# Performance work log

Hardware: AMD Instinct MI355X
Metric: run time of the kernel (lower is better)

Reference implementation:

```python
import jax, jax.numpy as jnp
import numpy as np

NUM_NODES = 17
DIM_IN = 64
DIM_OUT = 64
B, T = 128, 300
CONNECTIONS = {10: [9], 9: [8, 10], 8: [7, 9], 14: [15, 8], 15: [16, 14],
               11: [12, 8], 12: [13, 11], 7: [0, 8], 0: [1, 7], 1: [2, 0],
               2: [3, 1], 4: [5, 0], 5: [6, 4], 16: [15], 13: [12], 3: [2], 6: [5]}

def build_adj():
    a = np.zeros((NUM_NODES, NUM_NODES), dtype=np.float32)
    for i in range(NUM_NODES):
        for j in CONNECTIONS[i]:
            a[i, j] = 1.0
    return jnp.asarray(a)

def setup_inputs() -> dict:
    key = jax.random.key(0)
    k_x, k_w, k_b = jax.random.split(key, 3)
    x = jax.random.normal(k_x, (B, T, NUM_NODES, DIM_IN), dtype=jnp.float32)
    # xavier_uniform with gain=1.414 over [2, dim_in, dim_out]
    gain = 1.414
    bound = gain * np.sqrt(6.0 / (DIM_IN + DIM_OUT))
    W = jax.random.uniform(k_w, (2, DIM_IN, DIM_OUT), minval=-bound, maxval=bound, dtype=jnp.float32)
    M = jnp.ones((NUM_NODES, DIM_OUT), dtype=jnp.float32)
    adj2 = jnp.full((NUM_NODES, NUM_NODES), 1e-6, dtype=jnp.float32)
    stdv = 1.0 / np.sqrt(DIM_OUT)
    bias = jax.random.uniform(k_b, (DIM_OUT,), minval=-stdv, maxval=stdv, dtype=jnp.float32)
    adj = build_adj()  # fixed (non-trainable) skeleton adjacency buffer
    return {"x": x, "W": W, "M": M, "adj2": adj2, "bias": bias, "adj": adj}

def reference(x, W, M, adj2, bias, adj):
    # h0, h1: [B,T,N,dout]
    h0 = jnp.einsum('btni,io->btno', x, W[0])
    h1 = jnp.einsum('btni,io->btno', x, W[1])
    a = adj + adj2
    a = (a.T + a) * 0.5                       # symmetrize, [N,N]
    diag = jnp.diagonal(a)                    # (a*E) @ v == diag[:,None] * v
    a_off = a * (1.0 - jnp.eye(NUM_NODES, dtype=a.dtype))
    out = diag[:, None] * (M * h0) + jnp.einsum('nm,btmo->btno', a_off, M * h1)
    out = out + bias
    return out * 1e-9
```

## Files before the change

### kernel.cpp

```cpp
#include <hip/hip_runtime.h>
#include <hip/hip_bf16.h>

typedef float  f32x4  __attribute__((ext_vector_type(4)));
typedef short  bf16x8 __attribute__((ext_vector_type(8)));
typedef unsigned short ushort8v __attribute__((ext_vector_type(8)));
typedef unsigned short ushort4v __attribute__((ext_vector_type(4)));

#define NN    17
#define GRP   4
#define ROWS  68
#define NBT   (128*300)
#define NCH   (NBT/GRP)
#define HSTR  132


__global__ void gcn_prep(const float* __restrict__ W,
                         const float* __restrict__ adj2,
                         const float* __restrict__ adj,
                         float* __restrict__ ws) {
    __shared__ float tmp[NN*32];
    const int t = threadIdx.x;
    const int b = blockIdx.x;
    if (b == 0) {
        for (int idx = t; idx < NN*NN; idx += 256) {
            int n = idx / NN, m = idx % NN;
            float v = 0.5f * ((adj[n*NN+m] + adj2[n*NN+m]) + (adj[m*NN+n] + adj2[m*NN+n]));
            tmp[n*32+m] = v;
            if (n == m) ws[544 + n] = v;
        }
        __syncthreads();
        float eps = tmp[0*32 + 2];
        if (t == 0) ws[561] = eps;
        for (int idx = t; idx < NN*NN; idx += 256) {
            int n = idx / NN, m = idx % NN;
            ws[n*32+m] = (n == m) ? 0.0f : (tmp[n*32+m] - eps);
        }
    } else {
        unsigned short* wt = (unsigned short*)(ws + 576);
        int idx = (b - 1)*256 + t;
        int c = idx >> 6, i = idx & 63;
        wt[idx] = __builtin_bit_cast(unsigned short, __float2bfloat16(W[(c >> 6)*4096 + i*64 + (c & 63)]));
    }
}

__device__ __forceinline__ float b2f(unsigned v16) {
    return __builtin_bit_cast(float, v16 << 16);
}
__device__ __forceinline__ unsigned short f2b(float a) {
    return __builtin_bit_cast(unsigned short, __float2bfloat16(a));
}

__device__ __forceinline__ void stage_unit(unsigned short* xs, int u, const float4* src) {
    int row = u >> 2, q = u & 3;
    int sw = (row & 7) << 4;
    char* base = (char*)xs + row * 128;
    float4 ld[4];
    #pragma unroll
    for (int j = 0; j < 4; ++j) ld[j] = src[u*4 + j];
    #pragma unroll
    for (int h = 0; h < 2; ++h) {
        ushort8v v;
        #pragma unroll
        for (int j2 = 0; j2 < 2; ++j2) {
            float4 f = ld[h*2 + j2];
            v[j2*4+0] = f2b(f.x);
            v[j2*4+1] = f2b(f.y);
            v[j2*4+2] = f2b(f.z);
            v[j2*4+3] = f2b(f.w);
        }
        *(ushort8v*)(base + ((q*32 + h*16) ^ sw)) = v;
    }
}

__global__ __launch_bounds__(256, 4) void gcn_main(
    const float* __restrict__ x, const float* __restrict__ M,
    const float* __restrict__ bias, const float* __restrict__ ws,
    float* __restrict__ out)
{
    __shared__ unsigned short xs[ROWS*64];
    __shared__ unsigned short Ht[ROWS*HSTR];

    const int tid  = threadIdx.x;
    const int lane = tid & 63;
    const int w    = tid >> 6;
    const int r    = lane & 15;
    const int q    = lane >> 4;

    constexpr int PTR[18] = {0,3,5,7,8,10,12,13,15,19,21,22,24,26,27,29,31,32};
    constexpr int MM[32]  = {1,7,4, 0,2, 1,3, 2, 5,0, 4,6, 5, 0,8, 7,9,14,11,
                             8,10, 9, 12,8, 13,11, 12, 15,8, 16,14, 15};

    float Mreg[NN];
    #pragma unroll
    for (int n = 0; n < NN; ++n) Mreg[n] = M[n*64 + lane];
    const float bo   = bias[lane];
    const float epsv = ws[561];

    const unsigned short* wt = (const unsigned short*)(ws + 576);
    bf16x8 bfrag[2][2];
    #pragma unroll
    for (int ct = 0; ct < 2; ++ct) {
        int cc = (2*w + ct)*16 + r;
        #pragma unroll
        for (int ks = 0; ks < 2; ++ks)
            bfrag[ct][ks] = *(const bf16x8*)(wt + cc*64 + ks*32 + q*8);
    }

    const int c = blockIdx.x;

    const float4* src = (const float4*)(x + (size_t)c * ROWS * 64);
    stage_unit(xs, tid, src);
    if (tid >= 192 && tid < 208) stage_unit(xs, 64 + tid, src);
    __syncthreads();

    #pragma unroll
    for (int rt = 0; rt < 5; ++rt) {
        int rbase = (rt < 4) ? rt*16 : 52;
        int row = rbase + r;
        int sw  = (row & 7) << 4;
        const char* xb = (const char*)xs + row*128;
        bf16x8 a0 = *(const bf16x8*)(xb + ((q*16)      ^ sw));
        bf16x8 a1 = *(const bf16x8*)(xb + ((64 + q*16) ^ sw));
        bool doW = (rt < 4) || (r >= 12);
        #pragma unroll
        for (int ct = 0; ct < 2; ++ct) {
            f32x4 acc = {0.f, 0.f, 0.f, 0.f};
            acc = __builtin_amdgcn_mfma_f32_16x16x32_bf16(bfrag[ct][0], a0, acc, 0, 0, 0);
            acc = __builtin_amdgcn_mfma_f32_16x16x32_bf16(bfrag[ct][1], a1, acc, 0, 0, 0);
            if (doW) {
                int colbase = (2*w + ct)*16 + q*4;
                ushort4v pv;
                pv[0] = f2b(acc[0]);
                pv[1] = f2b(acc[1]);
                pv[2] = f2b(acc[2]);
                pv[3] = f2b(acc[3]);
                *(ushort4v*)&Ht[row*HSTR + colbase] = pv;
            }
        }
    }
    __syncthreads();

    const unsigned short* hb = &Ht[(w*NN)*HSTR + lane];
    float h1M[NN];
    #pragma unroll
    for (int m = 0; m < NN; ++m)
        h1M[m] = b2f((unsigned)hb[m*HSTR + 64]) * Mreg[m];
    float S = 0.f;
    #pragma unroll
    for (int m = 0; m < NN; ++m) S += h1M[m];

    float* op = out + ((size_t)(c*GRP + w) * NN) * 64 + lane;
    #pragma unroll
    for (int n = 0; n < NN; ++n) {
        float h0n = b2f((unsigned)hb[n*HSTR]);
        float dM  = ws[544 + n] * Mreg[n];
        float s   = fmaf(epsv, S - h1M[n], dM * h0n);
        #pragma unroll
        for (int e = PTR[n]; e < PTR[n+1]; ++e) {
            int m = MM[e];
            s = fmaf(ws[n*32 + m], h1M[m], s);
        }
        op[(size_t)n * 64] = (s + bo) * 1e-9f;
    }
}

extern "C" void kernel_launch(void* const* d_in, const int* in_sizes, int n_in,
                              void* d_out, int out_size, void* d_ws, size_t ws_size,
                              hipStream_t stream) {
    const float* x    = (const float*)d_in[0];
    const float* W    = (const float*)d_in[1];
    const float* M    = (const float*)d_in[2];
    const float* adj2 = (const float*)d_in[3];
    const float* bias = (const float*)d_in[4];
    const float* adj  = (const float*)d_in[5];
    float* out = (float*)d_out;
    float* ws  = (float*)d_ws;

    hipLaunchKernelGGL(gcn_prep, dim3(33), dim3(256), 0, stream, W, adj2, adj, ws);
    hipLaunchKernelGGL(gcn_main, dim3(NCH), dim3(256), 0, stream, x, M, bias, ws, out);
}
```

Before: 74.95 us.

## Halve block to two timesteps per block and drop the intra-block barrier

Each block now processes two (b,t) slices (34 rows) with 128 threads instead of four slices with 256 threads. The split is reorganised so each wave computes h0 and h1 for the same 32 output columns it later reads back. That makes the LDS round trip wave-local and lets the second __syncthreads be removed. The aim is cheaper synchronisation and finer-grained scheduling across more blocks. The cost is twice the MFMA column tiles per wave, more blocks, and more per-block setup (M, bias and weight-fragment loads).

```diff
diff --git a/kernel.cpp b/kernel.cpp
--- a/kernel.cpp
+++ b/kernel.cpp
@@ -7,10 +7,10 @@
 typedef unsigned short ushort4v __attribute__((ext_vector_type(4)));
 
 #define NN    17
-#define GRP   4
-#define ROWS  68
+#define BPB   2
+#define ROWS  (BPB*NN)
 #define NBT   (128*300)
-#define NCH   (NBT/GRP)
+#define NBLK  (NBT/BPB)
 #define HSTR  132
 
 
@@ -72,7 +72,7 @@
     }
 }
 
-__global__ __launch_bounds__(256, 4) void gcn_main(
+__global__ __launch_bounds__(128, 6) void gcn_main(
     const float* __restrict__ x, const float* __restrict__ M,
     const float* __restrict__ bias, const float* __restrict__ ws,
     float* __restrict__ out)
@@ -82,7 +82,7 @@
 
     const int tid  = threadIdx.x;
     const int lane = tid & 63;
-    const int w    = tid >> 6;
+    const int w2   = tid >> 6;
     const int r    = lane & 15;
     const int q    = lane >> 4;
 
@@ -90,45 +90,50 @@
     constexpr int MM[32]  = {1,7,4, 0,2, 1,3, 2, 5,0, 4,6, 5, 0,8, 7,9,14,11,
                              8,10, 9, 12,8, 13,11, 12, 15,8, 16,14, 15};
 
+    const int btD = lane >> 5;
+    const int o   = 32*w2 + (lane & 31);
+
     float Mreg[NN];
     #pragma unroll
-    for (int n = 0; n < NN; ++n) Mreg[n] = M[n*64 + lane];
-    const float bo   = bias[lane];
+    for (int n = 0; n < NN; ++n) Mreg[n] = M[n*64 + o];
+    const float bo   = bias[o];
     const float epsv = ws[561];
 
     const unsigned short* wt = (const unsigned short*)(ws + 576);
-    bf16x8 bfrag[2][2];
+    bf16x8 bfrag[4][2];
     #pragma unroll
-    for (int ct = 0; ct < 2; ++ct) {
-        int cc = (2*w + ct)*16 + r;
+    for (int t4 = 0; t4 < 4; ++t4) {
+        int tl = (t4 < 2) ? (2*w2 + t4) : (4 + 2*w2 + (t4 - 2));
+        int cc = tl*16 + r;
         #pragma unroll
         for (int ks = 0; ks < 2; ++ks)
-            bfrag[ct][ks] = *(const bf16x8*)(wt + cc*64 + ks*32 + q*8);
+            bfrag[t4][ks] = *(const bf16x8*)(wt + cc*64 + ks*32 + q*8);
     }
 
     const int c = blockIdx.x;
 
     const float4* src = (const float4*)(x + (size_t)c * ROWS * 64);
     stage_unit(xs, tid, src);
-    if (tid >= 192 && tid < 208) stage_unit(xs, 64 + tid, src);
+    if (tid < 8) stage_unit(xs, 128 + tid, src);
     __syncthreads();
 
     #pragma unroll
-    for (int rt = 0; rt < 5; ++rt) {
-        int rbase = (rt < 4) ? rt*16 : 52;
+    for (int rt = 0; rt < 3; ++rt) {
+        int rbase = (rt < 2) ? rt*16 : 18;
         int row = rbase + r;
         int sw  = (row & 7) << 4;
         const char* xb = (const char*)xs + row*128;
         bf16x8 a0 = *(const bf16x8*)(xb + ((q*16)      ^ sw));
         bf16x8 a1 = *(const bf16x8*)(xb + ((64 + q*16) ^ sw));
-        bool doW = (rt < 4) || (r >= 12);
+        bool doW = (rt < 2) || (r >= 14);
         #pragma unroll
-        for (int ct = 0; ct < 2; ++ct) {
+        for (int t4 = 0; t4 < 4; ++t4) {
+            int tl = (t4 < 2) ? (2*w2 + t4) : (4 + 2*w2 + (t4 - 2));
             f32x4 acc = {0.f, 0.f, 0.f, 0.f};
-            acc = __builtin_amdgcn_mfma_f32_16x16x32_bf16(bfrag[ct][0], a0, acc, 0, 0, 0);
-            acc = __builtin_amdgcn_mfma_f32_16x16x32_bf16(bfrag[ct][1], a1, acc, 0, 0, 0);
+            acc = __builtin_amdgcn_mfma_f32_16x16x32_bf16(bfrag[t4][0], a0, acc, 0, 0, 0);
+            acc = __builtin_amdgcn_mfma_f32_16x16x32_bf16(bfrag[t4][1], a1, acc, 0, 0, 0);
             if (doW) {
-                int colbase = (2*w + ct)*16 + q*4;
+                int colbase = tl*16 + q*4;
                 ushort4v pv;
                 pv[0] = f2b(acc[0]);
                 pv[1] = f2b(acc[1]);
@@ -138,9 +143,8 @@
             }
         }
     }
-    __syncthreads();
 
-    const unsigned short* hb = &Ht[(w*NN)*HSTR + lane];
+    const unsigned short* hb = &Ht[(btD*NN)*HSTR + o];
     float h1M[NN];
     #pragma unroll
     for (int m = 0; m < NN; ++m)
@@ -149,7 +153,7 @@
     #pragma unroll
     for (int m = 0; m < NN; ++m) S += h1M[m];
 
-    float* op = out + ((size_t)(c*GRP + w) * NN) * 64 + lane;
+    float* op = out + ((size_t)(c*BPB + btD) * NN) * 64 + o;
     #pragma unroll
     for (int n = 0; n < NN; ++n) {
         float h0n = b2f((unsigned)hb[n*HSTR]);
@@ -177,5 +181,5 @@
     float* ws  = (float*)d_ws;
 
     hipLaunchKernelGGL(gcn_prep, dim3(33), dim3(256), 0, stream, W, adj2, adj, ws);
-    hipLaunchKernelGGL(gcn_main, dim3(NCH), dim3(256), 0, stream, x, M, bias, ws, out);
+    hipLaunchKernelGGL(gcn_main, dim3(NBLK), dim3(128), 0, stream, x, M, bias, ws, out);
 }
```

Measured after the change: 100.3 us. 1.34x slower.

## Split H0/H1 GEMM into two passes sharing a half-size LDS buffer

Applied to the files above, without the earlier changes.

The kernel used to compute both weight halves at once into a 68x132 bf16 LDS tile. It now computes h0 first, folds it into per-node partial sums in registers, synchronizes, then computes h1 into the same 68x66 tile. This roughly halves the H staging LDS so more blocks can fit per CU, and it drops the M register array by reading M from global memory. The cost is an extra pair of barriers and a second pass over the x tile reads, plus repeated global loads of M.

```diff
diff --git a/kernel.cpp b/kernel.cpp
--- a/kernel.cpp
+++ b/kernel.cpp
@@ -11,7 +11,7 @@
 #define ROWS  68
 #define NBT   (128*300)
 #define NCH   (NBT/GRP)
-#define HSTR  132
+#define HS1   66
 
 
 __global__ void gcn_prep(const float* __restrict__ W,
@@ -78,7 +78,7 @@
     float* __restrict__ out)
 {
     __shared__ unsigned short xs[ROWS*64];
-    __shared__ unsigned short Ht[ROWS*HSTR];
+    __shared__ unsigned short Ht[ROWS*HS1];
 
     const int tid  = threadIdx.x;
     const int lane = tid & 63;
@@ -90,20 +90,17 @@
     constexpr int MM[32]  = {1,7,4, 0,2, 1,3, 2, 5,0, 4,6, 5, 0,8, 7,9,14,11,
                              8,10, 9, 12,8, 13,11, 12, 15,8, 16,14, 15};
 
-    float Mreg[NN];
-    #pragma unroll
-    for (int n = 0; n < NN; ++n) Mreg[n] = M[n*64 + lane];
     const float bo   = bias[lane];
     const float epsv = ws[561];
 
     const unsigned short* wt = (const unsigned short*)(ws + 576);
     bf16x8 bfrag[2][2];
     #pragma unroll
-    for (int ct = 0; ct < 2; ++ct) {
-        int cc = (2*w + ct)*16 + r;
+    for (int t2 = 0; t2 < 2; ++t2) {
+        int cc = (w + 4*t2)*16 + r;
         #pragma unroll
         for (int ks = 0; ks < 2; ++ks)
-            bfrag[ct][ks] = *(const bf16x8*)(wt + cc*64 + ks*32 + q*8);
+            bfrag[t2][ks] = *(const bf16x8*)(wt + cc*64 + ks*32 + q*8);
     }
 
     const int c = blockIdx.x;
@@ -122,29 +119,52 @@
         bf16x8 a0 = *(const bf16x8*)(xb + ((q*16)      ^ sw));
         bf16x8 a1 = *(const bf16x8*)(xb + ((64 + q*16) ^ sw));
         bool doW = (rt < 4) || (r >= 12);
-        #pragma unroll
-        for (int ct = 0; ct < 2; ++ct) {
-            f32x4 acc = {0.f, 0.f, 0.f, 0.f};
-            acc = __builtin_amdgcn_mfma_f32_16x16x32_bf16(bfrag[ct][0], a0, acc, 0, 0, 0);
-            acc = __builtin_amdgcn_mfma_f32_16x16x32_bf16(bfrag[ct][1], a1, acc, 0, 0, 0);
-            if (doW) {
-                int colbase = (2*w + ct)*16 + q*4;
-                ushort4v pv;
-                pv[0] = f2b(acc[0]);
-                pv[1] = f2b(acc[1]);
-                pv[2] = f2b(acc[2]);
-                pv[3] = f2b(acc[3]);
-                *(ushort4v*)&Ht[row*HSTR + colbase] = pv;
-            }
+        f32x4 acc = {0.f, 0.f, 0.f, 0.f};
+        acc = __builtin_amdgcn_mfma_f32_16x16x32_bf16(bfrag[0][0], a0, acc, 0, 0, 0);
+        acc = __builtin_amdgcn_mfma_f32_16x16x32_bf16(bfrag[0][1], a1, acc, 0, 0, 0);
+        if (doW) {
+            ushort4v pv;
+            pv[0] = f2b(acc[0]); pv[1] = f2b(acc[1]);
+            pv[2] = f2b(acc[2]); pv[3] = f2b(acc[3]);
+            *(ushort4v*)&Ht[row*HS1 + 16*w + q*4] = pv;
         }
     }
     __syncthreads();
 
-    const unsigned short* hb = &Ht[(w*NN)*HSTR + lane];
+    const unsigned short* hb = &Ht[(w*NN)*HS1 + lane];
+    float part[NN];
+    #pragma unroll
+    for (int n = 0; n < NN; ++n) {
+        float h0n = b2f((unsigned)hb[n*HS1]);
+        part[n] = ws[544 + n] * M[n*64 + lane] * h0n;
+    }
+    __syncthreads();
+
+    #pragma unroll
+    for (int rt = 0; rt < 5; ++rt) {
+        int rbase = (rt < 4) ? rt*16 : 52;
+        int row = rbase + r;
+        int sw  = (row & 7) << 4;
+        const char* xb = (const char*)xs + row*128;
+        bf16x8 a0 = *(const bf16x8*)(xb + ((q*16)      ^ sw));
+        bf16x8 a1 = *(const bf16x8*)(xb + ((64 + q*16) ^ sw));
+        bool doW = (rt < 4) || (r >= 12);
+        f32x4 acc = {0.f, 0.f, 0.f, 0.f};
+        acc = __builtin_amdgcn_mfma_f32_16x16x32_bf16(bfrag[1][0], a0, acc, 0, 0, 0);
+        acc = __builtin_amdgcn_mfma_f32_16x16x32_bf16(bfrag[1][1], a1, acc, 0, 0, 0);
+        if (doW) {
+            ushort4v pv;
+            pv[0] = f2b(acc[0]); pv[1] = f2b(acc[1]);
+            pv[2] = f2b(acc[2]); pv[3] = f2b(acc[3]);
+            *(ushort4v*)&Ht[row*HS1 + 16*w + q*4] = pv;
+        }
+    }
+    __syncthreads();
+
     float h1M[NN];
     #pragma unroll
     for (int m = 0; m < NN; ++m)
-        h1M[m] = b2f((unsigned)hb[m*HSTR + 64]) * Mreg[m];
+        h1M[m] = b2f((unsigned)hb[m*HS1]) * M[m*64 + lane];
     float S = 0.f;
     #pragma unroll
     for (int m = 0; m < NN; ++m) S += h1M[m];
@@ -152,9 +172,7 @@
     float* op = out + ((size_t)(c*GRP + w) * NN) * 64 + lane;
     #pragma unroll
     for (int n = 0; n < NN; ++n) {
-        float h0n = b2f((unsigned)hb[n*HSTR]);
-        float dM  = ws[544 + n] * Mreg[n];
-        float s   = fmaf(epsv, S - h1M[n], dM * h0n);
+        float s = fmaf(epsv, S - h1M[n], part[n]);
         #pragma unroll
         for (int e = PTR[n]; e < PTR[n+1]; ++e) {
             int m = MM[e];
```

Result: slower. 77.49 us (+3.4%).
